# Kernel tuning notes

Measured on AMD Instinct MI355X. Metric: run time of the kernel, lower is better.

Reference implementation:

```python
import jax, jax.numpy as jnp
import numpy as np

HEADS = 8
AGENT = 49
POOL = 7   # sqrt(AGENT)
WIN = 32


def _adaptive_avg_pool(x, out):
    # x: (b, h, w, c) -> (b, out, out, c), replicating torch AdaptiveAvgPool2d bins
    h = x.shape[1]
    starts = [(i * h) // out for i in range(out)]
    ends = [-((-(i + 1) * h) // out) for i in range(out)]
    rows = jnp.stack([x[:, s:e].mean(axis=1) for s, e in zip(starts, ends)], axis=1)      # (b,out,w,c)
    return jnp.stack([rows[:, :, s:e].mean(axis=2) for s, e in zip(starts, ends)], axis=2)  # (b,out,out,c)


def setup_inputs() -> dict:
    key = jax.random.key(0)
    ks = jax.random.split(key, 13)
    b, n, c = 32, WIN * WIN, 256
    std = 0.02
    return {
        "x": jax.random.normal(ks[0], (b, n + 1, c), jnp.float32),
        "qkv_w": jax.random.normal(ks[1], (3 * c, c), jnp.float32) * std,
        "proj_w": jax.random.normal(ks[2], (c, c), jnp.float32) * std,
        "proj_b": jnp.zeros((c,), jnp.float32),
        "dwc_w": jax.random.normal(ks[3], (c, 1, 3, 3), jnp.float32) * std,  # torch (C_out, 1, kh, kw)
        "dwc_b": jnp.zeros((c,), jnp.float32),
        "an_bias": jax.random.normal(ks[4], (HEADS, AGENT, 7, 7), jnp.float32) * std,
        "ah_bias": jax.random.normal(ks[5], (1, HEADS, AGENT, WIN, 1), jnp.float32) * std,
        "aw_bias": jax.random.normal(ks[6], (1, HEADS, AGENT, 1, WIN), jnp.float32) * std,
        "na_bias": jax.random.normal(ks[7], (HEADS, AGENT, 7, 7), jnp.float32) * std,
        "ha_bias": jax.random.normal(ks[8], (1, HEADS, WIN, 1, AGENT), jnp.float32) * std,
        "wa_bias": jax.random.normal(ks[9], (1, HEADS, 1, WIN, AGENT), jnp.float32) * std,
    }


def reference(x, qkv_w, proj_w, proj_b, dwc_w, dwc_b,
              an_bias, ah_bias, aw_bias, na_bias, ha_bias, wa_bias):
    cls_tok, xs = x[:, :1], x[:, 1:]
    b, n, c = xs.shape
    h = w = WIN
    hd = c // HEADS
    scale = hd ** -0.5

    qkv = xs @ qkv_w.T                                   # (b, n, 3c)
    q, k, v = jnp.split(qkv, 3, axis=-1)                 # each (b, n, c)

    # agent tokens: adaptive avg pool of q over the spatial grid
    agents = _adaptive_avg_pool(q.reshape(b, h, w, c), POOL).reshape(b, AGENT, c)

    qh = q.reshape(b, n, HEADS, hd).transpose(0, 2, 1, 3)        # (b,H,n,d)
    kh = k.reshape(b, n, HEADS, hd).transpose(0, 2, 1, 3)
    vh = v.reshape(b, n, HEADS, hd).transpose(0, 2, 1, 3)
    ah = agents.reshape(b, AGENT, HEADS, hd).transpose(0, 2, 1, 3)  # (b,H,A,d)

    # stage 1: agent <-> k/v, bias interpolated 7x7 -> WINxWIN (half-pixel bilinear == torch align_corners=False)
    pb1 = jax.image.resize(an_bias, (HEADS, AGENT, WIN, WIN), method='bilinear').reshape(1, HEADS, AGENT, n)
    pb2 = (ah_bias + aw_bias).reshape(1, HEADS, AGENT, n)
    agent_attn = jax.nn.softmax((ah * scale) @ kh.transpose(0, 1, 3, 2) + pb1 + pb2, axis=-1)  # (b,H,A,n)
    agent_v = agent_attn @ vh                                    # (b,H,A,d)

    # stage 2: q <-> agents
    ab1 = jax.image.resize(na_bias, (HEADS, AGENT, WIN, WIN), method='bilinear').reshape(1, HEADS, AGENT, n).transpose(0, 1, 3, 2)
    ab2 = (ha_bias + wa_bias).reshape(1, HEADS, n, AGENT)
    q_attn = jax.nn.softmax((qh * scale) @ ah.transpose(0, 1, 3, 2) + ab1 + ab2, axis=-1)      # (b,H,n,A)
    out = (q_attn @ agent_v).transpose(0, 2, 1, 3).reshape(b, n, c)

    # depthwise conv residual on v (NHWC)
    v_img = vh.transpose(0, 2, 1, 3).reshape(b, h, w, c)
    kern = dwc_w.transpose(2, 3, 1, 0)                            # (3,3,1,c) HWIO
    dwc = jax.lax.conv_general_dilated(v_img, kern, (1, 1), 'SAME',
                                       feature_group_count=c,
                                       dimension_numbers=('NHWC', 'HWIO', 'NHWC')) + dwc_b
    out = out + dwc.reshape(b, n, c)

    out = jnp.concatenate([cls_tok, out], axis=1)
    return out @ proj_w.T + proj_b
```

## Files before the change

kernel.cpp:

```cpp
#include <hip/hip_runtime.h>
#include <hip/hip_bf16.h>

#define BATCH 32
#define NTOK 1024
#define CH 256
#define HEADS 8
#define HD 32
#define AGENTS 49
#define WIN 32
#define QKV_N 768
#define SCALE 0.17677669529663687f

typedef unsigned short u16;
typedef __attribute__((ext_vector_type(8))) unsigned short u16x8;
typedef __attribute__((ext_vector_type(8))) short short8;
typedef __attribute__((ext_vector_type(4))) float f32x4;

__device__ __forceinline__ void gload_lds16(const void* g, const void* l) {
    __builtin_amdgcn_global_load_lds(
        (const __attribute__((address_space(1))) unsigned int*)g,
        (__attribute__((address_space(3))) unsigned int*)l, 16, 0, 0);
}

__device__ __forceinline__ u16 f2bf1(float f) {
    unsigned u = __builtin_bit_cast(unsigned, f);
    u += 0x7fffu + ((u >> 16) & 1u);
    return (u16)(u >> 16);
}
__device__ __forceinline__ float bf2f(u16 v) {
    unsigned u = ((unsigned)v) << 16;
    return __builtin_bit_cast(float, u);
}

__global__ void f2bf_kernel(const float* __restrict__ in, u16* __restrict__ out, int n8) {
    int i = blockIdx.x * 256 + threadIdx.x;
    if (i >= n8) return;
    float4 v0 = ((const float4*)in)[i * 2];
    float4 v1 = ((const float4*)in)[i * 2 + 1];
    u16x8 o;
    o[0] = f2bf1(v0.x); o[1] = f2bf1(v0.y); o[2] = f2bf1(v0.z); o[3] = f2bf1(v0.w);
    o[4] = f2bf1(v1.x); o[5] = f2bf1(v1.y); o[6] = f2bf1(v1.z); o[7] = f2bf1(v1.w);
    ((u16x8*)out)[i] = o;
}

__global__ __launch_bounds__(256) void gemm_bf16(const u16* __restrict__ A,
                                                 const u16* __restrict__ B,
                                                 float* __restrict__ C,
                                                 u16* __restrict__ C16,
                                                 int M, int N, int K,
                                                 const float* __restrict__ bias,
                                                 int amode) {
    __shared__ u16 As[128 * 32];
    __shared__ u16 Bs[128 * 32];
    const int tid = threadIdx.x;
    const int lane = tid & 63;
    const int wid = tid >> 6;
    const int row0 = blockIdx.x * 128, col0 = blockIdx.y * 128;
    const int wr = wid >> 1, wc = wid & 1;
    const int fr = lane & 15, fq = lane >> 4;

    f32x4 acc[4][4];
#pragma unroll
    for (int m = 0; m < 4; ++m)
#pragma unroll
        for (int n = 0; n < 4; ++n) acc[m][n] = (f32x4)(0.f);

    for (int k0 = 0; k0 < K; k0 += 32) {
#pragma unroll
        for (int r = 0; r < 2; ++r) {
            int trow = (tid >> 2) + r * 64;
            int tcol = (tid & 3) * 8;
            size_t aoff;
            int grow = row0 + trow;
            if (amode == 1) {
                int bb = grow >> 10, nn = grow & 1023;
                aoff = ((size_t)(bb * 1025 + nn + 1)) * 256 + (size_t)(k0 + tcol);
            } else {
                if (grow >= M) grow = M - 1;
                aoff = (size_t)grow * K + (size_t)(k0 + tcol);
            }
            gload_lds16(A + aoff, (const char*)As + wid * 1024 + r * 4096);
            int brow = col0 + trow;
            gload_lds16(B + (size_t)brow * K + (size_t)(k0 + tcol),
                        (const char*)Bs + wid * 1024 + r * 4096);
        }
        __syncthreads();

        short8 af[4], bf[4];
#pragma unroll
        for (int m = 0; m < 4; ++m)
            af[m] = *(const short8*)&As[(wr * 64 + m * 16 + fr) * 32 + fq * 8];
#pragma unroll
        for (int n = 0; n < 4; ++n)
            bf[n] = *(const short8*)&Bs[(wc * 64 + n * 16 + fr) * 32 + fq * 8];
#pragma unroll
        for (int m = 0; m < 4; ++m)
#pragma unroll
            for (int n = 0; n < 4; ++n)
                acc[m][n] = __builtin_amdgcn_mfma_f32_16x16x32_bf16(af[m], bf[n], acc[m][n], 0, 0, 0);
        __syncthreads();
    }

#pragma unroll
    for (int m = 0; m < 4; ++m) {
#pragma unroll
        for (int j = 0; j < 4; ++j) {
            int row = row0 + wr * 64 + m * 16 + fq * 4 + j;
            if (row < M) {
#pragma unroll
                for (int n = 0; n < 4; ++n) {
                    int col = col0 + wc * 64 + n * 16 + fr;
                    float v = acc[m][n][j];
                    if (bias) v += bias[col];
                    if (C16) C16[(size_t)row * N + col] = f2bf1(v);
                    else     C[(size_t)row * N + col] = v;
                }
            }
        }
    }
}

__global__ __launch_bounds__(256) void pool_kernel(const u16* __restrict__ qkvb,
                                                   float* __restrict__ agents) {
    int b = blockIdx.x / 7, py = blockIdx.x % 7;
    int ch = threadIdx.x;
    int ys = py * 32 / 7, ye = ((py + 1) * 32 + 6) / 7;
    float acc[7];
#pragma unroll
    for (int i = 0; i < 7; ++i) acc[i] = 0.f;
    for (int y = ys; y < ye; ++y) {
        const u16* rowp = qkvb + ((size_t)(b * NTOK + y * 32)) * QKV_N + ch;
#pragma unroll
        for (int PX = 0; PX < 7; ++PX) {
            const int xs = PX * 32 / 7, xe = ((PX + 1) * 32 + 6) / 7;
            float s = 0.f;
            for (int x = xs; x < xe; ++x) s += bf2f(rowp[(size_t)x * QKV_N]);
            acc[PX] += s;
        }
    }
    int rcnt = ye - ys;
#pragma unroll
    for (int PX = 0; PX < 7; ++PX) {
        const int xs = PX * 32 / 7, xe = ((PX + 1) * 32 + 6) / 7;
        agents[((size_t)(b * AGENTS + py * 7 + PX)) * CH + ch] =
            acc[PX] / (float)(rcnt * (xe - xs));
    }
}

__device__ inline float bilin7(const float* __restrict__ m, float sy, float sx) {
    float fy0 = floorf(sy), fx0 = floorf(sx);
    int y0 = (int)fy0, x0 = (int)fx0;
    float fy = sy - fy0, fx = sx - fx0;
    int y0c = min(max(y0, 0), 6), y1c = min(max(y0 + 1, 0), 6);
    int x0c = min(max(x0, 0), 6), x1c = min(max(x0 + 1, 0), 6);
    float v00 = m[y0c * 7 + x0c], v01 = m[y0c * 7 + x1c];
    float v10 = m[y1c * 7 + x0c], v11 = m[y1c * 7 + x1c];
    return (1.f - fy) * ((1.f - fx) * v00 + fx * v01) + fy * ((1.f - fx) * v10 + fx * v11);
}

__global__ void pb_kernel(const float* __restrict__ an, const float* __restrict__ ahb,
                          const float* __restrict__ awb, float* __restrict__ pba) {
    int h = blockIdx.x / AGENTS, a = blockIdx.x % AGENTS;
    const float* m = an + (h * AGENTS + a) * 49;
    for (int n = threadIdx.x; n < NTOK; n += 256) {
        int y = n >> 5, x = n & 31;
        float v = bilin7(m, (y + 0.5f) * (7.f / 32.f) - 0.5f, (x + 0.5f) * (7.f / 32.f) - 0.5f);
        v += ahb[(h * AGENTS + a) * 32 + y] + awb[(h * AGENTS + a) * 32 + x];
        pba[((size_t)(h * AGENTS + a)) * NTOK + n] = v;
    }
}

__global__ void ab_kernel(const float* __restrict__ na, const float* __restrict__ hab,
                          const float* __restrict__ wab, float* __restrict__ ab) {
    int idx = blockIdx.x * 256 + threadIdx.x;
    if (idx >= HEADS * NTOK * AGENTS) return;
    int h = idx / (NTOK * AGENTS);
    int r = idx % (NTOK * AGENTS);
    int n = r / AGENTS, a = r % AGENTS;
    int y = n >> 5, x = n & 31;
    const float* m = na + (h * AGENTS + a) * 49;
    float v = bilin7(m, (y + 0.5f) * (7.f / 32.f) - 0.5f, (x + 0.5f) * (7.f / 32.f) - 0.5f);
    v += hab[(h * 32 + y) * AGENTS + a] + wab[(h * 32 + x) * AGENTS + a];
    ab[idx] = v;
}

__global__ __launch_bounds__(512) void agent_attn3(const u16* __restrict__ qkvb,
                                                   const float* __restrict__ agents,
                                                   const float* __restrict__ pba,
                                                   float* __restrict__ agent_v) {
    int b = blockIdx.x >> 3, h = blockIdx.x & 7;
    int tid = threadIdx.x, lane = tid & 63, w = tid >> 6;
    const int fr = lane & 15, fq = lane >> 4;

#define VTP 1038
    __shared__ u16 ah_lds[64 * 32];
    __shared__ u16 Vt[32 * VTP];
    __shared__ float PO[8][2304];
    __shared__ float lsum_lds[8][64];

    u16*   Pw = (u16*)&PO[w][0];
    float* Ow = &PO[w][0];

    for (int li = tid; li < 64 * 32; li += 512) {
        int a = li >> 5, d = li & 31;
        float v = (a < AGENTS) ? agents[((size_t)(b * AGENTS + a)) * CH + h * HD + d] * SCALE : 0.f;
        ah_lds[li] = f2bf1(v);
    }
    for (int li = tid; li < NTOK * 4; li += 512) {
        int tok = li >> 2, d8 = (li & 3) * 8;
        u16x8 v = *(const u16x8*)&qkvb[((size_t)(b * NTOK + tok)) * QKV_N + 2 * CH + h * HD + d8];
#pragma unroll
        for (int j = 0; j < 8; ++j) Vt[(d8 + j) * VTP + tok] = v[j];
    }
    __syncthreads();

    short8 ahf[4];
#pragma unroll
    for (int mt = 0; mt < 4; ++mt)
        ahf[mt] = *(const short8*)&ah_lds[(mt * 16 + fr) * 32 + fq * 8];

    float lsum[4][4];
#pragma unroll
    for (int mt = 0; mt < 4; ++mt)
#pragma unroll
        for (int j = 0; j < 4; ++j) lsum[mt][j] = 0.f;
    f32x4 accO[4][2];
#pragma unroll
    for (int mt = 0; mt < 4; ++mt)
#pragma unroll
        for (int ntd = 0; ntd < 2; ++ntd) accO[mt][ntd] = (f32x4)(0.f);

    const float* pbh = pba + (size_t)h * AGENTS * NTOK;

#pragma unroll
    for (int c2 = 0; c2 < 2; ++c2) {
        int tb = w * 128 + c2 * 64;
        short8 kf[4];
#pragma unroll
        for (int nt = 0; nt < 4; ++nt)
            kf[nt] = *(const short8*)&qkvb[((size_t)(b * NTOK + tb + nt * 16 + fr)) * QKV_N + CH + h * HD + fq * 8];

        f32x4 accS[4];
#pragma unroll
        for (int mt = 0; mt < 4; ++mt) {
#pragma unroll
            for (int nt = 0; nt < 4; ++nt)
                accS[nt] = __builtin_amdgcn_mfma_f32_16x16x32_bf16(ahf[mt], kf[nt], (f32x4)(0.f), 0, 0, 0);
#pragma unroll
            for (int j = 0; j < 4; ++j) {
                int a = mt * 16 + fq * 4 + j;
                const float* pbrow = pbh + (size_t)min(a, AGENTS - 1) * NTOK + tb;
#pragma unroll
                for (int nt = 0; nt < 4; ++nt) {
                    float e = __expf(accS[nt][j] + pbrow[nt * 16 + fr]);
                    lsum[mt][j] += e;
                    Pw[a * 72 + nt * 16 + fr] = f2bf1(e);
                }
            }
        }

        asm volatile("s_waitcnt lgkmcnt(0)" ::: "memory");
        __builtin_amdgcn_sched_barrier(0);

        short8 pf[4][2], vf[2][2];
#pragma unroll
        for (int mt = 0; mt < 4; ++mt)
#pragma unroll
            for (int kc = 0; kc < 2; ++kc)
                pf[mt][kc] = *(const short8*)&Pw[(mt * 16 + fr) * 72 + kc * 32 + fq * 8];
#pragma unroll
        for (int ntd = 0; ntd < 2; ++ntd)
#pragma unroll
            for (int kc = 0; kc < 2; ++kc)
                vf[ntd][kc] = *(const short8*)&Vt[(ntd * 16 + fr) * VTP + tb + kc * 32 + fq * 8];

        asm volatile("s_waitcnt lgkmcnt(0)" ::: "memory");
        __builtin_amdgcn_sched_barrier(0);

#pragma unroll
        for (int mt = 0; mt < 4; ++mt)
#pragma unroll
            for (int kc = 0; kc < 2; ++kc)
#pragma unroll
                for (int ntd = 0; ntd < 2; ++ntd)
                    accO[mt][ntd] = __builtin_amdgcn_mfma_f32_16x16x32_bf16(pf[mt][kc], vf[ntd][kc], accO[mt][ntd], 0, 0, 0);
    }

#pragma unroll
    for (int mt = 0; mt < 4; ++mt)
#pragma unroll
        for (int j = 0; j < 4; ++j) {
            float s = lsum[mt][j];
            s += __shfl_xor(s, 1);
            s += __shfl_xor(s, 2);
            s += __shfl_xor(s, 4);
            s += __shfl_xor(s, 8);
            lsum[mt][j] = s;
        }
    if (fr == 0) {
#pragma unroll
        for (int mt = 0; mt < 4; ++mt)
#pragma unroll
            for (int j = 0; j < 4; ++j)
                lsum_lds[w][mt * 16 + fq * 4 + j] = lsum[mt][j];
    }

#pragma unroll
    for (int mt = 0; mt < 4; ++mt)
#pragma unroll
        for (int ntd = 0; ntd < 2; ++ntd)
#pragma unroll
            for (int j = 0; j < 4; ++j)
                Ow[(mt * 16 + fq * 4 + j) * 32 + ntd * 16 + fr] = accO[mt][ntd][j];

    asm volatile("s_waitcnt lgkmcnt(0)" ::: "memory");
    __syncthreads();

    for (int li = tid; li < AGENTS * HD; li += 512) {
        int a = li >> 5, d = li & 31;
        float L = 0.f, o = 0.f;
#pragma unroll
        for (int ww = 0; ww < 8; ++ww) {
            o += PO[ww][a * 32 + d];
            L += lsum_lds[ww][a];
        }
        agent_v[(((size_t)(b * HEADS + h)) * AGENTS + a) * HD + d] = o / L;
    }
#undef VTP
}

__global__ __launch_bounds__(256) void q_attn_dwc(const u16* __restrict__ qkvb,
                                                  const float* __restrict__ agents,
                                                  const float* __restrict__ agent_v,
                                                  const float* __restrict__ ab,
                                                  const float* __restrict__ dwc_w,
                                                  const float* __restrict__ dwc_b,
                                                  u16* __restrict__ outbf) {
    int blk = blockIdx.x;
    int b = blk / 32, rem = blk % 32;
    int h = rem / 4, ck = rem % 4;
    int tid = threadIdx.x;
    int w = tid >> 6, lane = tid & 63;
    int fr = lane & 15, fq = lane >> 4;
    int tb = ck * 256 + w * 64;
    int ylocal = tid >> 5, x = tid & 31;

    __shared__ u16 Vs[10][32][40];
    __shared__ u16 ah_lds[64][32];
    __shared__ u16 avT[32][72];
    __shared__ float PO[4][2304];
    __shared__ float w9[9][32];
    __shared__ float bia[32];

    u16*   Pw = (u16*)&PO[w][0];
    float* Ow = &PO[w][0];

    for (int li = tid; li < 64 * 32; li += 256) {
        int a = li >> 5, d = li & 31;
        float v = (a < AGENTS) ? agents[((size_t)(b * AGENTS + a)) * CH + h * HD + d] * SCALE : 0.f;
        ah_lds[a][d] = f2bf1(v);
    }
    for (int li = tid; li < 32 * 64; li += 256) {
        int d = li >> 6, a = li & 63;
        float v = (a < AGENTS) ? agent_v[(((size_t)(b * HEADS + h)) * AGENTS + a) * HD + d] : 0.f;
        avT[d][a] = f2bf1(v);
    }
    for (int li = tid; li < 288; li += 256) {
        int t = li >> 5, d = li & 31;
        w9[t][d] = dwc_w[(h * HD + d) * 9 + t];
    }
    if (tid < 32) bia[tid] = dwc_b[h * HD + tid];
    {
        int y0 = ck * 8 - 1;
#pragma unroll
        for (int it = 0; it < 5; ++it) {
            int c = it * 256 + tid;
            int r = c >> 7;
            int w7 = c & 127;
            int xx = w7 >> 2;
            int d8 = (w7 & 3) * 8;
            int yy = y0 + r;
            u16x8 v = (u16x8)(0);
            if (yy >= 0 && yy < 32)
                v = *(const u16x8*)&qkvb[((size_t)(b * NTOK + yy * 32 + xx)) * QKV_N + 2 * CH + h * HD + d8];
            *(u16x8*)&Vs[r][xx][d8] = v;
        }
    }
    __syncthreads();

    short8 ahf[4];
#pragma unroll
    for (int nt = 0; nt < 4; ++nt)
        ahf[nt] = *(const short8*)&ah_lds[nt * 16 + fr][fq * 8];

    const float* abh = ab + (size_t)h * NTOK * AGENTS;
#pragma unroll
    for (int mt = 0; mt < 4; ++mt) {
        int tok = tb + mt * 16 + fr;
        short8 qf = *(const short8*)(qkvb + ((size_t)(b * NTOK + tok)) * QKV_N + h * HD + fq * 8);
        f32x4 accS[4];
#pragma unroll
        for (int nt = 0; nt < 4; ++nt)
            accS[nt] = __builtin_amdgcn_mfma_f32_16x16x32_bf16(qf, ahf[nt], (f32x4)(0.f), 0, 0, 0);

        float e[4][4];
        float ps[4];
#pragma unroll
        for (int j = 0; j < 4; ++j) ps[j] = 0.f;
#pragma unroll
        for (int j = 0; j < 4; ++j) {
            int tkj = tb + mt * 16 + fq * 4 + j;
            const float* abrow = abh + (size_t)tkj * AGENTS;
#pragma unroll
            for (int nt = 0; nt < 4; ++nt) {
                int a = nt * 16 + fr;
                float s = accS[nt][j] + abrow[min(a, AGENTS - 1)];
                float ev = (a < AGENTS) ? __expf(s) : 0.f;
                e[j][nt] = ev;
                ps[j] += ev;
            }
        }
#pragma unroll
        for (int j = 0; j < 4; ++j) {
            ps[j] += __shfl_xor(ps[j], 1);
            ps[j] += __shfl_xor(ps[j], 2);
            ps[j] += __shfl_xor(ps[j], 4);
            ps[j] += __shfl_xor(ps[j], 8);
        }
#pragma unroll
        for (int j = 0; j < 4; ++j) {
            float inv = 1.f / ps[j];
            int tl = mt * 16 + fq * 4 + j;
#pragma unroll
            for (int nt = 0; nt < 4; ++nt)
                Pw[tl * 72 + nt * 16 + fr] = f2bf1(e[j][nt] * inv);
        }
    }

    asm volatile("s_waitcnt lgkmcnt(0)" ::: "memory");
    __builtin_amdgcn_sched_barrier(0);

    short8 avf[2][2], pf[4][2];
#pragma unroll
    for (int ntd = 0; ntd < 2; ++ntd)
#pragma unroll
        for (int c = 0; c < 2; ++c)
            avf[ntd][c] = *(const short8*)&avT[ntd * 16 + fr][c * 32 + fq * 8];
#pragma unroll
    for (int mt = 0; mt < 4; ++mt)
#pragma unroll
        for (int c = 0; c < 2; ++c)
            pf[mt][c] = *(const short8*)&Pw[(mt * 16 + fr) * 72 + c * 32 + fq * 8];

    asm volatile("s_waitcnt lgkmcnt(0)" ::: "memory");
    __builtin_amdgcn_sched_barrier(0);

    f32x4 accO[4][2];
#pragma unroll
    for (int mt = 0; mt < 4; ++mt)
#pragma unroll
        for (int ntd = 0; ntd < 2; ++ntd) accO[mt][ntd] = (f32x4)(0.f);
#pragma unroll
    for (int mt = 0; mt < 4; ++mt)
#pragma unroll
        for (int c = 0; c < 2; ++c)
#pragma unroll
            for (int ntd = 0; ntd < 2; ++ntd)
                accO[mt][ntd] = __builtin_amdgcn_mfma_f32_16x16x32_bf16(pf[mt][c], avf[ntd][c], accO[mt][ntd], 0, 0, 0);

#pragma unroll
    for (int mt = 0; mt < 4; ++mt)
#pragma unroll
        for (int ntd = 0; ntd < 2; ++ntd)
#pragma unroll
            for (int j = 0; j < 4; ++j)
                Ow[(mt * 16 + fq * 4 + j) * 36 + ntd * 16 + fr] = accO[mt][ntd][j];

    asm volatile("s_waitcnt lgkmcnt(0)" ::: "memory");
    __builtin_amdgcn_sched_barrier(0);

    int n = ck * 256 + tid;
    float o[HD];
#pragma unroll
    for (int c = 0; c < 8; ++c) {
        float4 t = *(const float4*)&Ow[lane * 36 + c * 4];
        o[c * 4 + 0] = t.x; o[c * 4 + 1] = t.y; o[c * 4 + 2] = t.z; o[c * 4 + 3] = t.w;
    }
#pragma unroll
    for (int d = 0; d < HD; ++d) o[d] += bia[d];
#pragma unroll
    for (int dy = -1; dy <= 1; ++dy) {
        int lr = ylocal + 1 + dy;
#pragma unroll
        for (int dx = -1; dx <= 1; ++dx) {
            int xx = x + dx;
            if (xx < 0 || xx > 31) continue;
            int t = (dy + 1) * 3 + (dx + 1);
            const u16* vrow = &Vs[lr][xx][0];
#pragma unroll
            for (int g = 0; g < 4; ++g) {
                u16x8 vv = *(const u16x8*)&vrow[g * 8];
                float4 w0 = *(const float4*)&w9[t][g * 8];
                float4 w1 = *(const float4*)&w9[t][g * 8 + 4];
                o[g * 8 + 0] = fmaf(w0.x, bf2f(vv[0]), o[g * 8 + 0]);
                o[g * 8 + 1] = fmaf(w0.y, bf2f(vv[1]), o[g * 8 + 1]);
                o[g * 8 + 2] = fmaf(w0.z, bf2f(vv[2]), o[g * 8 + 2]);
                o[g * 8 + 3] = fmaf(w0.w, bf2f(vv[3]), o[g * 8 + 3]);
                o[g * 8 + 4] = fmaf(w1.x, bf2f(vv[4]), o[g * 8 + 4]);
                o[g * 8 + 5] = fmaf(w1.y, bf2f(vv[5]), o[g * 8 + 5]);
                o[g * 8 + 6] = fmaf(w1.z, bf2f(vv[6]), o[g * 8 + 6]);
                o[g * 8 + 7] = fmaf(w1.w, bf2f(vv[7]), o[g * 8 + 7]);
            }
        }
    }

    u16* op = outbf + ((size_t)(b * 1025 + 1 + n)) * CH + h * HD;
#pragma unroll
    for (int g = 0; g < 4; ++g) {
        u16x8 pk;
#pragma unroll
        for (int j = 0; j < 8; ++j) pk[j] = f2bf1(o[g * 8 + j]);
        ((u16x8*)op)[g] = pk;
    }
}

extern "C" void kernel_launch(void* const* d_in, const int* in_sizes, int n_in,
                              void* d_out, int out_size, void* d_ws, size_t ws_size,
                              hipStream_t stream) {
    const float* x      = (const float*)d_in[0];
    const float* qkv_w  = (const float*)d_in[1];
    const float* proj_w = (const float*)d_in[2];
    const float* proj_b = (const float*)d_in[3];
    const float* dwc_w  = (const float*)d_in[4];
    const float* dwc_b  = (const float*)d_in[5];
    const float* an_b   = (const float*)d_in[6];
    const float* ah_b   = (const float*)d_in[7];
    const float* aw_b   = (const float*)d_in[8];
    const float* na_b   = (const float*)d_in[9];
    const float* ha_b   = (const float*)d_in[10];
    const float* wa_b   = (const float*)d_in[11];
    float* out = (float*)d_out;

    float* ws      = (float*)d_ws;
    u16*   qkvb    = (u16*)ws;
    float* agents  = ws + 12582912;
    float* pba     = agents + 401408;
    float* ab      = pba + 401408;
    float* agent_v = ab + 401408;
    u16* xbf  = (u16*)(agent_v + 401408);
    u16* qwbf = xbf + 8396800;
    u16* pwbf = qwbf + 196608;

    f2bf_kernel<<<4100, 256, 0, stream>>>(x, xbf, 8396800 / 8);
    f2bf_kernel<<<96, 256, 0, stream>>>(qkv_w, qwbf, 196608 / 8);
    f2bf_kernel<<<32, 256, 0, stream>>>(proj_w, pwbf, 65536 / 8);
    gemm_bf16<<<dim3(256, 6), 256, 0, stream>>>(xbf, qwbf, nullptr, qkvb, 32768, 768, 256, nullptr, 1);
    pool_kernel<<<BATCH * 7, 256, 0, stream>>>(qkvb, agents);
    pb_kernel<<<HEADS * AGENTS, 256, 0, stream>>>(an_b, ah_b, aw_b, pba);
    ab_kernel<<<(HEADS * NTOK * AGENTS + 255) / 256, 256, 0, stream>>>(na_b, ha_b, wa_b, ab);
    agent_attn3<<<BATCH * HEADS, 512, 0, stream>>>(qkvb, agents, pba, agent_v);
    q_attn_dwc<<<BATCH * HEADS * 4, 256, 0, stream>>>(qkvb, agents, agent_v, ab, dwc_w, dwc_b, xbf);
    gemm_bf16<<<dim3(257, 2), 256, 0, stream>>>(xbf, pwbf, out, nullptr, 32800, 256, 256, proj_b, 0);
}
```

Measured before the change: 145.7 us.

## Apply depthwise conv directly on MFMA accumulators, drop output LDS round-trip

The q_attn_dwc kernel now handles each wave's 64 tokens in two halves of 32 and keeps the P·V accumulators in registers. The depthwise conv residual and bias are added straight onto the MFMA output layout, so the fp32 staging buffer in shared memory and its transpose are gone, and the P buffer becomes smaller. This cuts LDS footprint and LDS traffic, which may raise occupancy. The cost is that output stores become scattered 2-byte writes per element instead of 16-byte vector stores, and V is read from LDS as scalars.

Measured after the change: 146.3 us. About the same (+0.4%).

```diff
diff --git a/kernel.cpp b/kernel.cpp
--- a/kernel.cpp
+++ b/kernel.cpp
@@ -343,17 +343,15 @@
     int w = tid >> 6, lane = tid & 63;
     int fr = lane & 15, fq = lane >> 4;
     int tb = ck * 256 + w * 64;
-    int ylocal = tid >> 5, x = tid & 31;
 
     __shared__ u16 Vs[10][32][40];
     __shared__ u16 ah_lds[64][32];
     __shared__ u16 avT[32][72];
-    __shared__ float PO[4][2304];
+    __shared__ u16 Pall[4][32 * 68];
     __shared__ float w9[9][32];
     __shared__ float bia[32];
 
-    u16*   Pw = (u16*)&PO[w][0];
-    float* Ow = &PO[w][0];
+    u16* Pw = &Pall[w][0];
 
     for (int li = tid; li < 64 * 32; li += 256) {
         int a = li >> 5, d = li & 31;
@@ -392,135 +390,121 @@
 #pragma unroll
     for (int nt = 0; nt < 4; ++nt)
         ahf[nt] = *(const short8*)&ah_lds[nt * 16 + fr][fq * 8];
+    short8 avf[2][2];
+#pragma unroll
+    for (int ntd = 0; ntd < 2; ++ntd)
+#pragma unroll
+        for (int kc = 0; kc < 2; ++kc)
+            avf[ntd][kc] = *(const short8*)&avT[ntd * 16 + fr][kc * 32 + fq * 8];
 
     const float* abh = ab + (size_t)h * NTOK * AGENTS;
-#pragma unroll
-    for (int mt = 0; mt < 4; ++mt) {
-        int tok = tb + mt * 16 + fr;
-        short8 qf = *(const short8*)(qkvb + ((size_t)(b * NTOK + tok)) * QKV_N + h * HD + fq * 8);
-        f32x4 accS[4];
-#pragma unroll
-        for (int nt = 0; nt < 4; ++nt)
-            accS[nt] = __builtin_amdgcn_mfma_f32_16x16x32_bf16(qf, ahf[nt], (f32x4)(0.f), 0, 0, 0);
-
-        float e[4][4];
-        float ps[4];
-#pragma unroll
-        for (int j = 0; j < 4; ++j) ps[j] = 0.f;
-#pragma unroll
-        for (int j = 0; j < 4; ++j) {
-            int tkj = tb + mt * 16 + fq * 4 + j;
-            const float* abrow = abh + (size_t)tkj * AGENTS;
-#pragma unroll
-            for (int nt = 0; nt < 4; ++nt) {
-                int a = nt * 16 + fr;
-                float s = accS[nt][j] + abrow[min(a, AGENTS - 1)];
-                float ev = (a < AGENTS) ? __expf(s) : 0.f;
-                e[j][nt] = ev;
-                ps[j] += ev;
-            }
-        }
-#pragma unroll
-        for (int j = 0; j < 4; ++j) {
-            ps[j] += __shfl_xor(ps[j], 1);
-            ps[j] += __shfl_xor(ps[j], 2);
-            ps[j] += __shfl_xor(ps[j], 4);
-            ps[j] += __shfl_xor(ps[j], 8);
-        }
-#pragma unroll
-        for (int j = 0; j < 4; ++j) {
-            float inv = 1.f / ps[j];
-            int tl = mt * 16 + fq * 4 + j;
+
+#pragma unroll
+    for (int half = 0; half < 2; ++half) {
+        int hb = tb + half * 32;
+
+#pragma unroll
+        for (int mt2 = 0; mt2 < 2; ++mt2) {
+            int tok = hb + mt2 * 16 + fr;
+            short8 qf = *(const short8*)(qkvb + ((size_t)(b * NTOK + tok)) * QKV_N + h * HD + fq * 8);
+            f32x4 accS[4];
 #pragma unroll
             for (int nt = 0; nt < 4; ++nt)
-                Pw[tl * 72 + nt * 16 + fr] = f2bf1(e[j][nt] * inv);
-        }
-    }
-
-    asm volatile("s_waitcnt lgkmcnt(0)" ::: "memory");
-    __builtin_amdgcn_sched_barrier(0);
-
-    short8 avf[2][2], pf[4][2];
-#pragma unroll
-    for (int ntd = 0; ntd < 2; ++ntd)
-#pragma unroll
-        for (int c = 0; c < 2; ++c)
-            avf[ntd][c] = *(const short8*)&avT[ntd * 16 + fr][c * 32 + fq * 8];
-#pragma unroll
-    for (int mt = 0; mt < 4; ++mt)
-#pragma unroll
-        for (int c = 0; c < 2; ++c)
-            pf[mt][c] = *(const short8*)&Pw[(mt * 16 + fr) * 72 + c * 32 + fq * 8];
-
-    asm volatile("s_waitcnt lgkmcnt(0)" ::: "memory");
-    __builtin_amdgcn_sched_barrier(0);
-
-    f32x4 accO[4][2];
-#pragma unroll
-    for (int mt = 0; mt < 4; ++mt)
-#pragma unroll
-        for (int ntd = 0; ntd < 2; ++ntd) accO[mt][ntd] = (f32x4)(0.f);
-#pragma unroll
-    for (int mt = 0; mt < 4; ++mt)
-#pragma unroll
-        for (int c = 0; c < 2; ++c)
-#pragma unroll
-            for (int ntd = 0; ntd < 2; ++ntd)
-                accO[mt][ntd] = __builtin_amdgcn_mfma_f32_16x16x32_bf16(pf[mt][c], avf[ntd][c], accO[mt][ntd], 0, 0, 0);
-
-#pragma unroll
-    for (int mt = 0; mt < 4; ++mt)
-#pragma unroll
-        for (int ntd = 0; ntd < 2; ++ntd)
-#pragma unroll
-            for (int j = 0; j < 4; ++j)
-                Ow[(mt * 16 + fq * 4 + j) * 36 + ntd * 16 + fr] = accO[mt][ntd][j];
-
-    asm volatile("s_waitcnt lgkmcnt(0)" ::: "memory");
-    __builtin_amdgcn_sched_barrier(0);
-
-    int n = ck * 256 + tid;
-    float o[HD];
-#pragma unroll
-    for (int c = 0; c < 8; ++c) {
-        float4 t = *(const float4*)&Ow[lane * 36 + c * 4];
-        o[c * 4 + 0] = t.x; o[c * 4 + 1] = t.y; o[c * 4 + 2] = t.z; o[c * 4 + 3] = t.w;
-    }
-#pragma unroll
-    for (int d = 0; d < HD; ++d) o[d] += bia[d];
-#pragma unroll
-    for (int dy = -1; dy <= 1; ++dy) {
-        int lr = ylocal + 1 + dy;
-#pragma unroll
-        for (int dx = -1; dx <= 1; ++dx) {
-            int xx = x + dx;
-            if (xx < 0 || xx > 31) continue;
-            int t = (dy + 1) * 3 + (dx + 1);
-            const u16* vrow = &Vs[lr][xx][0];
-#pragma unroll
-            for (int g = 0; g < 4; ++g) {
-                u16x8 vv = *(const u16x8*)&vrow[g * 8];
-                float4 w0 = *(const float4*)&w9[t][g * 8];
-                float4 w1 = *(const float4*)&w9[t][g * 8 + 4];
-                o[g * 8 + 0] = fmaf(w0.x, bf2f(vv[0]), o[g * 8 + 0]);
-                o[g * 8 + 1] = fmaf(w0.y, bf2f(vv[1]), o[g * 8 + 1]);
-                o[g * 8 + 2] = fmaf(w0.z, bf2f(vv[2]), o[g * 8 + 2]);
-                o[g * 8 + 3] = fmaf(w0.w, bf2f(vv[3]), o[g * 8 + 3]);
-                o[g * 8 + 4] = fmaf(w1.x, bf2f(vv[4]), o[g * 8 + 4]);
-                o[g * 8 + 5] = fmaf(w1.y, bf2f(vv[5]), o[g * 8 + 5]);
-                o[g * 8 + 6] = fmaf(w1.z, bf2f(vv[6]), o[g * 8 + 6]);
-                o[g * 8 + 7] = fmaf(w1.w, bf2f(vv[7]), o[g * 8 + 7]);
-            }
-        }
-    }
-
-    u16* op = outbf + ((size_t)(b * 1025 + 1 + n)) * CH + h * HD;
-#pragma unroll
-    for (int g = 0; g < 4; ++g) {
-        u16x8 pk;
-#pragma unroll
-        for (int j = 0; j < 8; ++j) pk[j] = f2bf1(o[g * 8 + j]);
-        ((u16x8*)op)[g] = pk;
+                accS[nt] = __builtin_amdgcn_mfma_f32_16x16x32_bf16(qf, ahf[nt], (f32x4)(0.f), 0, 0, 0);
+
+            float e[4][4];
+            float ps[4];
+#pragma unroll
+            for (int j = 0; j < 4; ++j) ps[j] = 0.f;
+#pragma unroll
+            for (int j = 0; j < 4; ++j) {
+                int tkj = hb + mt2 * 16 + fq * 4 + j;
+                const float* abrow = abh + (size_t)tkj * AGENTS;
+#pragma unroll
+                for (int nt = 0; nt < 4; ++nt) {
+                    int a = nt * 16 + fr;
+                    float s = accS[nt][j] + abrow[min(a, AGENTS - 1)];
+                    float ev = (a < AGENTS) ? __expf(s) : 0.f;
+                    e[j][nt] = ev;
+                    ps[j] += ev;
+                }
+            }
+#pragma unroll
+            for (int j = 0; j < 4; ++j) {
+                ps[j] += __shfl_xor(ps[j], 1);
+                ps[j] += __shfl_xor(ps[j], 2);
+                ps[j] += __shfl_xor(ps[j], 4);
+                ps[j] += __shfl_xor(ps[j], 8);
+            }
+#pragma unroll
+            for (int j = 0; j < 4; ++j) {
+                float inv = 1.f / ps[j];
+                int tl = mt2 * 16 + fq * 4 + j;
+#pragma unroll
+                for (int nt = 0; nt < 4; ++nt)
+                    Pw[tl * 68 + nt * 16 + fr] = f2bf1(e[j][nt] * inv);
+            }
+        }
+
+        asm volatile("s_waitcnt lgkmcnt(0)" ::: "memory");
+        __builtin_amdgcn_sched_barrier(0);
+
+        short8 pf[2][2];
+#pragma unroll
+        for (int mt2 = 0; mt2 < 2; ++mt2)
+#pragma unroll
+            for (int kc = 0; kc < 2; ++kc)
+                pf[mt2][kc] = *(const short8*)&Pw[(mt2 * 16 + fr) * 68 + kc * 32 + fq * 8];
+
+        asm volatile("s_waitcnt lgkmcnt(0)" ::: "memory");
+        __builtin_amdgcn_sched_barrier(0);
+
+        f32x4 accO[2][2];
+#pragma unroll
+        for (int mt2 = 0; mt2 < 2; ++mt2)
+#pragma unroll
+            for (int ntd = 0; ntd < 2; ++ntd) accO[mt2][ntd] = (f32x4)(0.f);
+#pragma unroll
+        for (int mt2 = 0; mt2 < 2; ++mt2)
+#pragma unroll
+            for (int kc = 0; kc < 2; ++kc)
+#pragma unroll
+                for (int ntd = 0; ntd < 2; ++ntd)
+                    accO[mt2][ntd] = __builtin_amdgcn_mfma_f32_16x16x32_bf16(pf[mt2][kc], avf[ntd][kc], accO[mt2][ntd], 0, 0, 0);
+
+        int y = ck * 8 + w * 2 + half;
+        int lr = w * 2 + half + 1;
+#pragma unroll
+        for (int ntd = 0; ntd < 2; ++ntd) {
+            int d = ntd * 16 + fr;
+            float wv[9];
+#pragma unroll
+            for (int t = 0; t < 9; ++t) wv[t] = w9[t][d];
+            float bv = bia[d];
+#pragma unroll
+            for (int mt2 = 0; mt2 < 2; ++mt2) {
+                int x0 = mt2 * 16 + fq * 4;
+                float vv[3][6];
+#pragma unroll
+                for (int dy = 0; dy < 3; ++dy)
+#pragma unroll
+                    for (int k = 0; k < 6; ++k) {
+                        int xx = x0 - 1 + k;
+                        vv[dy][k] = (xx >= 0 && xx < 32) ? bf2f(Vs[lr - 1 + dy][xx][d]) : 0.f;
+                    }
+#pragma unroll
+                for (int j = 0; j < 4; ++j) {
+                    float o = accO[mt2][ntd][j] + bv;
+#pragma unroll
+                    for (int dy = 0; dy < 3; ++dy)
+#pragma unroll
+                        for (int dx = 0; dx < 3; ++dx)
+                            o = fmaf(wv[dy * 3 + dx], vv[dy][j + dx], o);
+                    int n = y * 32 + x0 + j;
+                    outbf[((size_t)(b * 1025 + 1 + n)) * CH + h * HD + d] = f2bf1(o);
+                }
+            }
+        }
     }
 }
 
```
